# Optimization experiments

Measured on AMD Instinct MI355X. Metric: run time of the kernel, lower is better.

The kernel has to match this reference:

```python
import jax, jax.numpy as jnp
import numpy as np

N = 50000      # nodes
E = 800000     # edges (avg degree 16)
D_IN = 128
D_H = 128
D_OUT = 64
L = 3          # num_layers
NEG_SLOPE = 0.1


def setup_inputs() -> dict:
    key = jax.random.key(0)
    ks = jax.random.split(key, 8)
    s = 0.05
    return {
        "x": jax.random.normal(ks[0], (N, D_IN), jnp.float32),
        "edge_index": jax.random.randint(ks[1], (2, E), 0, N),
        # SAGEConv params per layer: lin_l (neighbors, with bias), lin_r (root)
        "wl": jax.random.normal(ks[2], (L, D_H, D_H), jnp.float32) * s,
        "wr": jax.random.normal(ks[3], (L, D_H, D_H), jnp.float32) * s,
        "bc": jnp.zeros((L, D_H), jnp.float32),
        # per-layer Linear params (first L-1 are hidden->hidden)
        "wlin": jax.random.normal(ks[4], (L - 1, D_H, D_H), jnp.float32) * s,
        "blin": jnp.zeros((L - 1, D_H), jnp.float32),
        # final Linear hidden->out
        "wout": jax.random.normal(ks[5], (D_H, D_OUT), jnp.float32) * s,
        "bout": jnp.zeros((D_OUT,), jnp.float32),
    }


def _sage_conv(x, src, dst, wl, wr, b):
    # mean aggregation of source features at destination nodes
    n = x.shape[0]
    agg = jax.ops.segment_sum(x[src], dst, num_segments=n)        # [N, d]
    cnt = jax.ops.segment_sum(jnp.ones((src.shape[0],), x.dtype), dst, num_segments=n)
    agg = agg / jnp.maximum(cnt, 1.0)[:, None]
    return agg @ wl + x @ wr + b


def _lrelu(v):
    return jnp.where(v > 0, v, NEG_SLOPE * v)


def reference(x, edge_index, wl, wr, bc, wlin, blin, wout, bout):
    src, dst = edge_index[0], edge_index[1]
    for i in range(L - 1):
        x = _lrelu(_sage_conv(x, src, dst, wl[i], wr[i], bc[i]))
        x = _lrelu(x @ wlin[i] + blin[i])
    x = _sage_conv(x, src, dst, wl[L - 1], wr[L - 1], bc[L - 1])
    return x @ wout + bout
```

## Files before the change

kernel.cpp:

```cpp
#include <hip/hip_runtime.h>

#define NEG_SLOPE 0.1f

typedef __bf16 bf16x8 __attribute__((ext_vector_type(8)));
typedef float f32x4 __attribute__((ext_vector_type(4)));
typedef unsigned int uint32x4 __attribute__((ext_vector_type(4)));
typedef unsigned short ushort;

__device__ inline ushort f2bf(float f) {
    unsigned int u = __float_as_uint(f);
    u += 0x7fffu + ((u >> 16) & 1u);
    return (ushort)(u >> 16);
}
__device__ inline float bf2f(ushort h) { return __uint_as_float(((unsigned int)h) << 16); }

__device__ inline void pack8(const float* v, uint32x4& hv, uint32x4& lv) {
    ushort hi[8], lo[8];
#pragma unroll
    for (int j = 0; j < 8; j++) {
        float f = v[j];
        ushort h = f2bf(f);
        hi[j] = h;
        lo[j] = f2bf(f - bf2f(h));
    }
    hv.x = hi[0] | ((unsigned)hi[1] << 16); hv.y = hi[2] | ((unsigned)hi[3] << 16);
    hv.z = hi[4] | ((unsigned)hi[5] << 16); hv.w = hi[6] | ((unsigned)hi[7] << 16);
    lv.x = lo[0] | ((unsigned)lo[1] << 16); lv.y = lo[2] | ((unsigned)lo[3] << 16);
    lv.z = lo[4] | ((unsigned)lo[5] << 16); lv.w = lo[6] | ((unsigned)lo[7] << 16);
}

__device__ inline void acc8(const uint32x4 u, float* a) {
    a[0] += __uint_as_float(u.x << 16); a[1] += __uint_as_float(u.x & 0xffff0000u);
    a[2] += __uint_as_float(u.y << 16); a[3] += __uint_as_float(u.y & 0xffff0000u);
    a[4] += __uint_as_float(u.z << 16); a[5] += __uint_as_float(u.z & 0xffff0000u);
    a[6] += __uint_as_float(u.w << 16); a[7] += __uint_as_float(u.w & 0xffff0000u);
}

__global__ void k_count(const int* __restrict__ ei, int E, int* __restrict__ degp,
                        int* __restrict__ rank) {
    int e = blockIdx.x * 256 + threadIdx.x;
    if (e < E) rank[e] = atomicAdd(&degp[(size_t)ei[E + e] * 16], 1);
}

__global__ void k_starts(const int* __restrict__ degp, int N, int* __restrict__ start,
                         int* __restrict__ deg, int* __restrict__ counter) {
    int n = blockIdx.x * 256 + threadIdx.x;
    int lane = threadIdx.x & 63;
    int d = (n < N) ? degp[(size_t)n * 16] : 0;
    int inc = d;
#pragma unroll
    for (int o = 1; o < 64; o <<= 1) {
        int v = __shfl_up(inc, o);
        if (lane >= o) inc += v;
    }
    int total = __shfl(inc, 63);
    int base = 0;
    if (lane == 0) base = atomicAdd(counter, total);
    base = __shfl(base, 0);
    int st = base + inc - d;
    if (n < N) { start[n] = st; deg[n] = d; }
}

__global__ void k_fill(const int* __restrict__ ei, int E, const int* __restrict__ start,
                       const int* __restrict__ rank, int* __restrict__ adj) {
    int e = blockIdx.x * 256 + threadIdx.x;
    if (e < E) {
        int s = ei[e];
        int dv = ei[E + e];
        adj[start[dv] + rank[e]] = s;
    }
}


__global__ __launch_bounds__(256) void k_wpack(const float* __restrict__ wl,
                                               const float* __restrict__ wr,
                                               const float* __restrict__ wlin,
                                               const float* __restrict__ wout,
                                               ushort* __restrict__ wph,
                                               ushort* __restrict__ wpl) {
    int m = blockIdx.y;
    int c = blockIdx.x * 256 + threadIdx.x;
    const float* src;
    int Nn = 128;
    size_t dstoff;
    if (m < 3)      { src = wl   + (size_t)m * 16384;       dstoff = (size_t)m * 16384; }
    else if (m < 6) { src = wr   + (size_t)(m - 3) * 16384; dstoff = (size_t)m * 16384; }
    else if (m < 8) { src = wlin + (size_t)(m - 6) * 16384; dstoff = (size_t)m * 16384; }
    else            { src = wout; Nn = 64;                  dstoff = (size_t)8 * 16384; }
    if (c >= Nn * 16) return;
    int cb = c >> 8, gg = (c >> 4) & 15, col = c & 15;
    float v[8];
#pragma unroll
    for (int j = 0; j < 8; j++)
        v[j] = src[(size_t)(gg * 8 + j) * Nn + cb * 16 + col];
    uint32x4 hv, lv;
    pack8(v, hv, lv);
    *(uint32x4*)(wph + dstoff + (size_t)c * 8) = hv;
    *(uint32x4*)(wpl + dstoff + (size_t)c * 8) = lv;
}


__global__ __launch_bounds__(256) void k_splitx(const float* __restrict__ x,
                                                ushort* __restrict__ oh,
                                                ushort* __restrict__ ol, int N) {
    int t = blockIdx.x * 256 + threadIdx.x;
    int row = t >> 4, g = t & 15;
    if (row >= N) return;
    const float* src = x + (size_t)row * 128 + g * 8;
    float v[8];
#pragma unroll
    for (int j = 0; j < 8; j++) v[j] = src[j];
    uint32x4 hv, lv;
    pack8(v, hv, lv);
    size_t off = (size_t)row * 128 + g * 8;
    *(uint32x4*)(oh + off) = hv;
    *(uint32x4*)(ol + off) = lv;
}


template <bool ACT1, int NM2, bool ACT2, bool FINAL>
__global__ __launch_bounds__(256) void k_fused(
    const ushort* __restrict__ hh,   const ushort* __restrict__ hl,
    const int* __restrict__ adj, const int* __restrict__ start,
    const int* __restrict__ deg,
    const ushort* __restrict__ w1h,  const ushort* __restrict__ w1l,
    const ushort* __restrict__ w2h,  const ushort* __restrict__ w2l,
    const float* __restrict__ b1,
    const ushort* __restrict__ w3h,  const ushort* __restrict__ w3l,
    const float* __restrict__ b2,
    ushort* __restrict__ oh, ushort* __restrict__ ol,
    float* __restrict__ of, int N) {
    constexpr int NCF2 = NM2 / 64;
    __shared__ ushort th[32][136];
    __shared__ ushort tl[32][136];

    const int tid = threadIdx.x;
    const int w = tid >> 6, lane = tid & 63;
    const int g = lane >> 4, r16 = lane & 15;
    const int m0 = blockIdx.x * 32;

    {
        const int qw = tid >> 4;
        const int q = tid & 15;
#pragma unroll
        for (int rep = 0; rep < 2; rep++) {
            int nr = qw + rep * 16;
            int node = m0 + nr;
            if (node > N - 1) node = N - 1;
            const int st = start[node], cnt = deg[node];
            const int h = cnt >> 1;
            const int stB = st + h;
            float a[8] = {0, 0, 0, 0, 0, 0, 0, 0};
            float b[8] = {0, 0, 0, 0, 0, 0, 0, 0};
            int i = 0;
            for (; i + 4 <= h; i += 4) {
                int s0 = adj[st + i], s1 = adj[st + i + 1];
                int s2 = adj[st + i + 2], s3 = adj[st + i + 3];
                int t0 = adj[stB + i], t1 = adj[stB + i + 1];
                int t2 = adj[stB + i + 2], t3 = adj[stB + i + 3];
                uint32x4 u0 = *(const uint32x4*)(hh + (size_t)s0 * 128 + q * 8);
                uint32x4 u1 = *(const uint32x4*)(hh + (size_t)s1 * 128 + q * 8);
                uint32x4 u2 = *(const uint32x4*)(hh + (size_t)s2 * 128 + q * 8);
                uint32x4 u3 = *(const uint32x4*)(hh + (size_t)s3 * 128 + q * 8);
                uint32x4 v0 = *(const uint32x4*)(hh + (size_t)t0 * 128 + q * 8);
                uint32x4 v1 = *(const uint32x4*)(hh + (size_t)t1 * 128 + q * 8);
                uint32x4 v2 = *(const uint32x4*)(hh + (size_t)t2 * 128 + q * 8);
                uint32x4 v3 = *(const uint32x4*)(hh + (size_t)t3 * 128 + q * 8);
                acc8(u0, a); acc8(u1, a); acc8(u2, a); acc8(u3, a);
                acc8(v0, b); acc8(v1, b); acc8(v2, b); acc8(v3, b);
            }
            const int im = i;
            for (; i < h; i++) {
                int s0 = adj[st + i];
                uint32x4 u = *(const uint32x4*)(hh + (size_t)s0 * 128 + q * 8);
                acc8(u, a);
            }
            for (int j = stB + im; j < st + cnt; j++) {
                int t0 = adj[j];
                uint32x4 u = *(const uint32x4*)(hh + (size_t)t0 * 128 + q * 8);
                acc8(u, b);
            }
            float inv = 1.0f / fmaxf((float)cnt, 1.0f);
            float v[8];
#pragma unroll
            for (int c = 0; c < 8; c++) v[c] = (a[c] + b[c]) * inv;
            uint32x4 hv, lv;
            pack8(v, hv, lv);
            *(uint32x4*)&th[nr][q * 8] = hv;
            *(uint32x4*)&tl[nr][q * 8] = lv;
        }
    }
    __syncthreads();

    size_t ro[2];
#pragma unroll
    for (int rf = 0; rf < 2; rf++) {
        int row = m0 + rf * 16 + r16;
        if (row > N - 1) row = N - 1;
        ro[rf] = (size_t)row * 128 + g * 8;
    }

    f32x4 acc[2][2];
#pragma unroll
    for (int rf = 0; rf < 2; rf++)
#pragma unroll
        for (int cf = 0; cf < 2; cf++) acc[rf][cf] = (f32x4){0.f, 0.f, 0.f, 0.f};

#pragma unroll
    for (int s = 0; s < 4; s++) {
        bf16x8 a1h_[2], a1l_[2], a2h_[2], a2l_[2];
#pragma unroll
        for (int rf = 0; rf < 2; rf++) {
            a1h_[rf] = *(const bf16x8*)&th[rf * 16 + r16][s * 32 + g * 8];
            a1l_[rf] = *(const bf16x8*)&tl[rf * 16 + r16][s * 32 + g * 8];
            a2h_[rf] = *(const bf16x8*)(hh + ro[rf] + s * 32);
            a2l_[rf] = *(const bf16x8*)(hl + ro[rf] + s * 32);
        }
        bf16x8 b1h_[2], b1l_[2], b2h_[2], b2l_[2];
#pragma unroll
        for (int cf = 0; cf < 2; cf++) {
            size_t o = (size_t)(w * 2 + cf) * 2048 + s * 512 + g * 128 + r16 * 8;
            b1h_[cf] = *(const bf16x8*)(w1h + o);
            b1l_[cf] = *(const bf16x8*)(w1l + o);
            b2h_[cf] = *(const bf16x8*)(w2h + o);
            b2l_[cf] = *(const bf16x8*)(w2l + o);
        }
#pragma unroll
        for (int rf = 0; rf < 2; rf++)
#pragma unroll
            for (int cf = 0; cf < 2; cf++) {
                acc[rf][cf] = __builtin_amdgcn_mfma_f32_16x16x32_bf16(a1h_[rf], b1h_[cf], acc[rf][cf], 0, 0, 0);
                acc[rf][cf] = __builtin_amdgcn_mfma_f32_16x16x32_bf16(a1h_[rf], b1l_[cf], acc[rf][cf], 0, 0, 0);
                acc[rf][cf] = __builtin_amdgcn_mfma_f32_16x16x32_bf16(a1l_[rf], b1h_[cf], acc[rf][cf], 0, 0, 0);
                acc[rf][cf] = __builtin_amdgcn_mfma_f32_16x16x32_bf16(a2h_[rf], b2h_[cf], acc[rf][cf], 0, 0, 0);
                acc[rf][cf] = __builtin_amdgcn_mfma_f32_16x16x32_bf16(a2h_[rf], b2l_[cf], acc[rf][cf], 0, 0, 0);
                acc[rf][cf] = __builtin_amdgcn_mfma_f32_16x16x32_bf16(a2l_[rf], b2h_[cf], acc[rf][cf], 0, 0, 0);
            }
    }
    __syncthreads();

    {
        float bv1[2];
#pragma unroll
        for (int cf = 0; cf < 2; cf++) bv1[cf] = b1[(w * 2 + cf) * 16 + r16];
#pragma unroll
        for (int rf = 0; rf < 2; rf++)
#pragma unroll
            for (int cf = 0; cf < 2; cf++)
#pragma unroll
                for (int i = 0; i < 4; i++) {
                    float v = acc[rf][cf][i] + bv1[cf];
                    if (ACT1) v = v > 0.f ? v : NEG_SLOPE * v;
                    ushort hi = f2bf(v);
                    ushort lo = f2bf(v - bf2f(hi));
                    th[rf * 16 + g * 4 + i][w * 32 + cf * 16 + r16] = hi;
                    tl[rf * 16 + g * 4 + i][w * 32 + cf * 16 + r16] = lo;
                }
    }
    __syncthreads();

    f32x4 acc2[2][NCF2];
#pragma unroll
    for (int rf = 0; rf < 2; rf++)
#pragma unroll
        for (int cf = 0; cf < NCF2; cf++) acc2[rf][cf] = (f32x4){0.f, 0.f, 0.f, 0.f};

#pragma unroll
    for (int s = 0; s < 4; s++) {
        bf16x8 ah_[2], al_[2];
#pragma unroll
        for (int rf = 0; rf < 2; rf++) {
            ah_[rf] = *(const bf16x8*)&th[rf * 16 + r16][s * 32 + g * 8];
            al_[rf] = *(const bf16x8*)&tl[rf * 16 + r16][s * 32 + g * 8];
        }
        bf16x8 wh_[NCF2], wlo_[NCF2];
#pragma unroll
        for (int cf = 0; cf < NCF2; cf++) {
            size_t o = (size_t)(w * NCF2 + cf) * 2048 + s * 512 + g * 128 + r16 * 8;
            wh_[cf] = *(const bf16x8*)(w3h + o);
            wlo_[cf] = *(const bf16x8*)(w3l + o);
        }
#pragma unroll
        for (int rf = 0; rf < 2; rf++)
#pragma unroll
            for (int cf = 0; cf < NCF2; cf++) {
                acc2[rf][cf] = __builtin_amdgcn_mfma_f32_16x16x32_bf16(ah_[rf], wh_[cf], acc2[rf][cf], 0, 0, 0);
                acc2[rf][cf] = __builtin_amdgcn_mfma_f32_16x16x32_bf16(ah_[rf], wlo_[cf], acc2[rf][cf], 0, 0, 0);
                acc2[rf][cf] = __builtin_amdgcn_mfma_f32_16x16x32_bf16(al_[rf], wh_[cf], acc2[rf][cf], 0, 0, 0);
            }
    }

    if constexpr (FINAL) {
        float bv2 = b2[w * 16 + r16];
#pragma unroll
        for (int rf = 0; rf < 2; rf++)
#pragma unroll
            for (int i = 0; i < 4; i++) {
                int row = m0 + rf * 16 + g * 4 + i;
                if (row < N) of[(size_t)row * 64 + w * 16 + r16] = acc2[rf][0][i] + bv2;
            }
    } else {
        __syncthreads();
        float bv2[2];
#pragma unroll
        for (int cf = 0; cf < 2; cf++) bv2[cf] = b2[(w * 2 + cf) * 16 + r16];
#pragma unroll
        for (int rf = 0; rf < 2; rf++)
#pragma unroll
            for (int cf = 0; cf < 2; cf++)
#pragma unroll
                for (int i = 0; i < 4; i++) {
                    float v = acc2[rf][cf][i] + bv2[cf];
                    if (ACT2) v = v > 0.f ? v : NEG_SLOPE * v;
                    ushort hi = f2bf(v);
                    ushort lo = f2bf(v - bf2f(hi));
                    th[rf * 16 + g * 4 + i][w * 32 + cf * 16 + r16] = hi;
                    tl[rf * 16 + g * 4 + i][w * 32 + cf * 16 + r16] = lo;
                }
        __syncthreads();
#pragma unroll
        for (int rep = 0; rep < 2; rep++) {
            int id = rep * 256 + tid;
            int row = id >> 4, kg = id & 15;
            int grow = m0 + row;
            if (grow < N) {
                uint32x4 hv = *(const uint32x4*)&th[row][kg * 8];
                uint32x4 lv = *(const uint32x4*)&tl[row][kg * 8];
                *(uint32x4*)(oh + (size_t)grow * 128 + kg * 8) = hv;
                *(uint32x4*)(ol + (size_t)grow * 128 + kg * 8) = lv;
            }
        }
    }
}


extern "C" void kernel_launch(void* const* d_in, const int* in_sizes, int n_in,
                              void* d_out, int out_size, void* d_ws, size_t ws_size,
                              hipStream_t stream) {
    const float* x    = (const float*)d_in[0];
    const int*   ei   = (const int*)d_in[1];
    const float* wl   = (const float*)d_in[2];
    const float* wr   = (const float*)d_in[3];
    const float* bc   = (const float*)d_in[4];
    const float* wlin = (const float*)d_in[5];
    const float* blin = (const float*)d_in[6];
    const float* wout = (const float*)d_in[7];
    const float* bout = (const float*)d_in[8];
    float* out = (float*)d_out;

    const int N = in_sizes[0] / 128;
    const int E = in_sizes[1] / 2;

    char* p = (char*)d_ws;
    auto alloc = [&](size_t bytes) {
        char* r = p;
        p += (bytes + 255) & ~(size_t)255;
        return r;
    };
    int* counter = (int*)alloc(4);
    int* degp    = (int*)alloc((size_t)N * 16 * 4);
    int* deg     = (int*)alloc((size_t)N * 4);
    int* start   = (int*)alloc((size_t)N * 4);
    int* rank    = (int*)alloc((size_t)E * 4);
    int* adj     = (int*)alloc((size_t)E * 4);
    ushort* wph  = (ushort*)alloc((size_t)139264 * 2);
    ushort* wpl  = (ushort*)alloc((size_t)139264 * 2);
    ushort* xh   = (ushort*)alloc((size_t)N * 128 * 2);
    ushort* xl   = (ushort*)alloc((size_t)N * 128 * 2);
    ushort* hAh  = (ushort*)alloc((size_t)N * 128 * 2);
    ushort* hAl  = (ushort*)alloc((size_t)N * 128 * 2);

    hipMemsetAsync(d_ws, 0, (size_t)((char*)(degp + (size_t)N * 16) - (char*)d_ws), stream);

    const int gE = (E + 255) / 256;
    const int gN = (N + 255) / 256;
    const int gQ = (N * 16 + 255) / 256;
    const int gF = (N + 31) / 32;

    k_count <<<gE, 256, 0, stream>>>(ei, E, degp, rank);
    k_starts<<<gN, 256, 0, stream>>>(degp, N, start, deg, counter);
    k_fill  <<<gE, 256, 0, stream>>>(ei, E, start, rank, adj);
    k_wpack <<<dim3(8, 9), 256, 0, stream>>>(wl, wr, wlin, wout, wph, wpl);
    k_splitx<<<gQ, 256, 0, stream>>>(x, xh, xl, N);

    const ushort *wl0h = wph,           *wl0l = wpl;
    const ushort *wl1h = wph + 16384,   *wl1l = wpl + 16384;
    const ushort *wl2h = wph + 32768,   *wl2l = wpl + 32768;
    const ushort *wr0h = wph + 3*16384, *wr0l = wpl + 3*16384;
    const ushort *wr1h = wph + 4*16384, *wr1l = wpl + 4*16384;
    const ushort *wr2h = wph + 5*16384, *wr2l = wpl + 5*16384;
    const ushort *wn0h = wph + 6*16384, *wn0l = wpl + 6*16384;
    const ushort *wn1h = wph + 7*16384, *wn1l = wpl + 7*16384;
    const ushort *woh  = wph + 8*16384, *wol  = wpl + 8*16384;

    k_fused<true, 128, true, false><<<gF, 256, 0, stream>>>(
        xh, xl, adj, start, deg, wl0h, wl0l, wr0h, wr0l, bc,
        wn0h, wn0l, blin, hAh, hAl, nullptr, N);
    k_fused<true, 128, true, false><<<gF, 256, 0, stream>>>(
        hAh, hAl, adj, start, deg, wl1h, wl1l, wr1h, wr1l, bc + 128,
        wn1h, wn1l, blin + 128, xh, xl, nullptr, N);
    k_fused<false, 64, false, true><<<gF, 256, 0, stream>>>(
        xh, xl, adj, start, deg, wl2h, wl2l, wr2h, wr2l, bc + 256,
        woh, wol, bout, nullptr, nullptr, out, N);
}
```

Before: 327.9 us.

## Split neighbor aggregation into a column-sliced kernel separate from the GEMM layer

Moves the mean-aggregation gather out of the fused layer kernel into its own kernel. The new kernel uses a 2D grid where each block covers 16 feature columns for 128 nodes, so concurrently running blocks touch a narrower slice of the feature matrix, which should improve cache hit rates on the random gathers. The aggregated hi/lo bf16 result is written to a new global buffer that the layer kernel then reads in place of shared memory. The cost is an extra round trip through global memory for the aggregate, three extra kernel launches, and adjacency indices re-read eight times.

```diff
diff --git a/kernel.cpp b/kernel.cpp
--- a/kernel.cpp
+++ b/kernel.cpp
@@ -70,7 +70,6 @@
         adj[start[dv] + rank[e]] = s;
     }
 }
-
 
 __global__ __launch_bounds__(256) void k_wpack(const float* __restrict__ wl,
                                                const float* __restrict__ wr,
@@ -99,7 +98,6 @@
     *(uint32x4*)(wpl + dstoff + (size_t)c * 8) = lv;
 }
 
-
 __global__ __launch_bounds__(256) void k_splitx(const float* __restrict__ x,
                                                 ushort* __restrict__ oh,
                                                 ushort* __restrict__ ol, int N) {
@@ -117,12 +115,61 @@
     *(uint32x4*)(ol + off) = lv;
 }
 
+__global__ __launch_bounds__(256) void k_agg_cs(const ushort* __restrict__ hh,
+                                                const int* __restrict__ adj,
+                                                const int* __restrict__ start,
+                                                const int* __restrict__ deg,
+                                                ushort* __restrict__ oh,
+                                                ushort* __restrict__ ol, int N) {
+    const int node = blockIdx.y * 128 + (threadIdx.x >> 1);
+    if (node >= N) return;
+    const int co = blockIdx.x * 16 + (threadIdx.x & 1) * 8;
+    const int st = start[node], cnt = deg[node];
+    const int h = cnt >> 1, stB = st + h;
+    float a[8] = {0, 0, 0, 0, 0, 0, 0, 0};
+    float b[8] = {0, 0, 0, 0, 0, 0, 0, 0};
+    int i = 0;
+    for (; i + 4 <= h; i += 4) {
+        int s0 = adj[st + i], s1 = adj[st + i + 1];
+        int s2 = adj[st + i + 2], s3 = adj[st + i + 3];
+        int t0 = adj[stB + i], t1 = adj[stB + i + 1];
+        int t2 = adj[stB + i + 2], t3 = adj[stB + i + 3];
+        uint32x4 u0 = *(const uint32x4*)(hh + (size_t)s0 * 128 + co);
+        uint32x4 u1 = *(const uint32x4*)(hh + (size_t)s1 * 128 + co);
+        uint32x4 u2 = *(const uint32x4*)(hh + (size_t)s2 * 128 + co);
+        uint32x4 u3 = *(const uint32x4*)(hh + (size_t)s3 * 128 + co);
+        uint32x4 v0 = *(const uint32x4*)(hh + (size_t)t0 * 128 + co);
+        uint32x4 v1 = *(const uint32x4*)(hh + (size_t)t1 * 128 + co);
+        uint32x4 v2 = *(const uint32x4*)(hh + (size_t)t2 * 128 + co);
+        uint32x4 v3 = *(const uint32x4*)(hh + (size_t)t3 * 128 + co);
+        acc8(u0, a); acc8(u1, a); acc8(u2, a); acc8(u3, a);
+        acc8(v0, b); acc8(v1, b); acc8(v2, b); acc8(v3, b);
+    }
+    const int im = i;
+    for (; i < h; i++) {
+        int s0 = adj[st + i];
+        uint32x4 u = *(const uint32x4*)(hh + (size_t)s0 * 128 + co);
+        acc8(u, a);
+    }
+    for (int j = stB + im; j < st + cnt; j++) {
+        int t0 = adj[j];
+        uint32x4 u = *(const uint32x4*)(hh + (size_t)t0 * 128 + co);
+        acc8(u, b);
+    }
+    float inv = 1.0f / fmaxf((float)cnt, 1.0f);
+    float v[8];
+#pragma unroll
+    for (int c = 0; c < 8; c++) v[c] = (a[c] + b[c]) * inv;
+    uint32x4 hv, lv;
+    pack8(v, hv, lv);
+    *(uint32x4*)(oh + (size_t)node * 128 + co) = hv;
+    *(uint32x4*)(ol + (size_t)node * 128 + co) = lv;
+}
 
 template <bool ACT1, int NM2, bool ACT2, bool FINAL>
-__global__ __launch_bounds__(256) void k_fused(
+__global__ __launch_bounds__(256) void k_layer(
+    const ushort* __restrict__ aggh, const ushort* __restrict__ aggl,
     const ushort* __restrict__ hh,   const ushort* __restrict__ hl,
-    const int* __restrict__ adj, const int* __restrict__ start,
-    const int* __restrict__ deg,
     const ushort* __restrict__ w1h,  const ushort* __restrict__ w1l,
     const ushort* __restrict__ w2h,  const ushort* __restrict__ w2l,
     const float* __restrict__ b1,
@@ -139,59 +186,6 @@
     const int g = lane >> 4, r16 = lane & 15;
     const int m0 = blockIdx.x * 32;
 
-    {
-        const int qw = tid >> 4;
-        const int q = tid & 15;
-#pragma unroll
-        for (int rep = 0; rep < 2; rep++) {
-            int nr = qw + rep * 16;
-            int node = m0 + nr;
-            if (node > N - 1) node = N - 1;
-            const int st = start[node], cnt = deg[node];
-            const int h = cnt >> 1;
-            const int stB = st + h;
-            float a[8] = {0, 0, 0, 0, 0, 0, 0, 0};
-            float b[8] = {0, 0, 0, 0, 0, 0, 0, 0};
-            int i = 0;
-            for (; i + 4 <= h; i += 4) {
-                int s0 = adj[st + i], s1 = adj[st + i + 1];
-                int s2 = adj[st + i + 2], s3 = adj[st + i + 3];
-                int t0 = adj[stB + i], t1 = adj[stB + i + 1];
-                int t2 = adj[stB + i + 2], t3 = adj[stB + i + 3];
-                uint32x4 u0 = *(const uint32x4*)(hh + (size_t)s0 * 128 + q * 8);
-                uint32x4 u1 = *(const uint32x4*)(hh + (size_t)s1 * 128 + q * 8);
-                uint32x4 u2 = *(const uint32x4*)(hh + (size_t)s2 * 128 + q * 8);
-                uint32x4 u3 = *(const uint32x4*)(hh + (size_t)s3 * 128 + q * 8);
-                uint32x4 v0 = *(const uint32x4*)(hh + (size_t)t0 * 128 + q * 8);
-                uint32x4 v1 = *(const uint32x4*)(hh + (size_t)t1 * 128 + q * 8);
-                uint32x4 v2 = *(const uint32x4*)(hh + (size_t)t2 * 128 + q * 8);
-                uint32x4 v3 = *(const uint32x4*)(hh + (size_t)t3 * 128 + q * 8);
-                acc8(u0, a); acc8(u1, a); acc8(u2, a); acc8(u3, a);
-                acc8(v0, b); acc8(v1, b); acc8(v2, b); acc8(v3, b);
-            }
-            const int im = i;
-            for (; i < h; i++) {
-                int s0 = adj[st + i];
-                uint32x4 u = *(const uint32x4*)(hh + (size_t)s0 * 128 + q * 8);
-                acc8(u, a);
-            }
-            for (int j = stB + im; j < st + cnt; j++) {
-                int t0 = adj[j];
-                uint32x4 u = *(const uint32x4*)(hh + (size_t)t0 * 128 + q * 8);
-                acc8(u, b);
-            }
-            float inv = 1.0f / fmaxf((float)cnt, 1.0f);
-            float v[8];
-#pragma unroll
-            for (int c = 0; c < 8; c++) v[c] = (a[c] + b[c]) * inv;
-            uint32x4 hv, lv;
-            pack8(v, hv, lv);
-            *(uint32x4*)&th[nr][q * 8] = hv;
-            *(uint32x4*)&tl[nr][q * 8] = lv;
-        }
-    }
-    __syncthreads();
-
     size_t ro[2];
 #pragma unroll
     for (int rf = 0; rf < 2; rf++) {
@@ -211,10 +205,11 @@
         bf16x8 a1h_[2], a1l_[2], a2h_[2], a2l_[2];
 #pragma unroll
         for (int rf = 0; rf < 2; rf++) {
-            a1h_[rf] = *(const bf16x8*)&th[rf * 16 + r16][s * 32 + g * 8];
-            a1l_[rf] = *(const bf16x8*)&tl[rf * 16 + r16][s * 32 + g * 8];
-            a2h_[rf] = *(const bf16x8*)(hh + ro[rf] + s * 32);
-            a2l_[rf] = *(const bf16x8*)(hl + ro[rf] + s * 32);
+            size_t o = ro[rf] + s * 32;
+            a1h_[rf] = *(const bf16x8*)(aggh + o);
+            a1l_[rf] = *(const bf16x8*)(aggl + o);
+            a2h_[rf] = *(const bf16x8*)(hh + o);
+            a2l_[rf] = *(const bf16x8*)(hl + o);
         }
         bf16x8 b1h_[2], b1l_[2], b2h_[2], b2l_[2];
 #pragma unroll
@@ -237,7 +232,6 @@
                 acc[rf][cf] = __builtin_amdgcn_mfma_f32_16x16x32_bf16(a2l_[rf], b2h_[cf], acc[rf][cf], 0, 0, 0);
             }
     }
-    __syncthreads();
 
     {
         float bv1[2];
@@ -369,6 +363,8 @@
     ushort* xl   = (ushort*)alloc((size_t)N * 128 * 2);
     ushort* hAh  = (ushort*)alloc((size_t)N * 128 * 2);
     ushort* hAl  = (ushort*)alloc((size_t)N * 128 * 2);
+    ushort* aggh = (ushort*)alloc((size_t)N * 128 * 2);
+    ushort* aggl = (ushort*)alloc((size_t)N * 128 * 2);
 
     hipMemsetAsync(d_ws, 0, (size_t)((char*)(degp + (size_t)N * 16) - (char*)d_ws), stream);
 
@@ -376,6 +372,7 @@
     const int gN = (N + 255) / 256;
     const int gQ = (N * 16 + 255) / 256;
     const int gF = (N + 31) / 32;
+    const dim3 gA(8, (N + 127) / 128);
 
     k_count <<<gE, 256, 0, stream>>>(ei, E, degp, rank);
     k_starts<<<gN, 256, 0, stream>>>(degp, N, start, deg, counter);
@@ -393,13 +390,16 @@
     const ushort *wn1h = wph + 7*16384, *wn1l = wpl + 7*16384;
     const ushort *woh  = wph + 8*16384, *wol  = wpl + 8*16384;
 
-    k_fused<true, 128, true, false><<<gF, 256, 0, stream>>>(
-        xh, xl, adj, start, deg, wl0h, wl0l, wr0h, wr0l, bc,
+    k_agg_cs<<<gA, 256, 0, stream>>>(xh, adj, start, deg, aggh, aggl, N);
+    k_layer<true, 128, true, false><<<gF, 256, 0, stream>>>(
+        aggh, aggl, xh, xl, wl0h, wl0l, wr0h, wr0l, bc,
         wn0h, wn0l, blin, hAh, hAl, nullptr, N);
-    k_fused<true, 128, true, false><<<gF, 256, 0, stream>>>(
-        hAh, hAl, adj, start, deg, wl1h, wl1l, wr1h, wr1l, bc + 128,
+    k_agg_cs<<<gA, 256, 0, stream>>>(hAh, adj, start, deg, aggh, aggl, N);
+    k_layer<true, 128, true, false><<<gF, 256, 0, stream>>>(
+        aggh, aggl, hAh, hAl, wl1h, wl1l, wr1h, wr1l, bc + 128,
         wn1h, wn1l, blin + 128, xh, xl, nullptr, N);
-    k_fused<false, 64, false, true><<<gF, 256, 0, stream>>>(
-        xh, xl, adj, start, deg, wl2h, wl2l, wr2h, wr2l, bc + 256,
+    k_agg_cs<<<gA, 256, 0, stream>>>(xh, adj, start, deg, aggh, aggl, N);
+    k_layer<false, 64, false, true><<<gF, 256, 0, stream>>>(
+        aggh, aggl, xh, xl, wl2h, wl2l, wr2h, wr2l, bc + 256,
         woh, wol, bout, nullptr, nullptr, out, N);
 }
```

Measured after the change: 517.7 us. 1.58x slower.
